# Performance work log

Hardware: AMD Instinct MI355X
Metric: run time of the kernel (lower is better)

## Reference

```python
import jax, jax.numpy as jnp
import numpy as np

B, S, DIM = 4, 4096, 1024
BASE_COUPLING = 0.1
NUM_CYCLES = 3


def _gelu(x):
    # torch nn.GELU default = exact erf formulation
    return jax.nn.gelu(x, approximate=False)


def setup_inputs() -> dict:
    key = jax.random.key(0)
    ks = jax.random.split(key, 9)
    d = DIM

    def w(k, fan_in, fan_out):
        return (jax.random.normal(k, (fan_in, fan_out), dtype=jnp.float32)
                / np.sqrt(fan_in).astype(np.float32))

    inp = {"x": jax.random.normal(ks[0], (B, S, d), dtype=jnp.float32)}
    # coupling_net: dim -> dim -> dim/2 -> dim/4 -> 1
    cn_dims = [(d, d), (d, d // 2), (d // 2, d // 4), (d // 4, 1)]
    for i, (a, b) in enumerate(cn_dims):
        inp[f"cn_w{i+1}"] = w(ks[1 + i], a, b)
        inp[f"cn_b{i+1}"] = jnp.zeros((b,), dtype=jnp.float32)
    # global_context_net: dim -> dim/2 -> dim/4 -> 1
    gc_dims = [(d, d // 2), (d // 2, d // 4), (d // 4, 1)]
    for i, (a, b) in enumerate(gc_dims):
        inp[f"gc_w{i+1}"] = w(ks[5 + i], a, b)
        inp[f"gc_b{i+1}"] = jnp.zeros((b,), dtype=jnp.float32)
    inp["adaptive_range"] = jnp.full((1,), 0.2, dtype=jnp.float32)
    return inp


def _coupling_net(h, w1, b1, w2, b2, w3, b3, w4, b4):
    h = _gelu(h @ w1 + b1)
    h = _gelu(h @ w2 + b2)
    h = _gelu(h @ w3 + b3)
    return jax.nn.sigmoid(h @ w4 + b4)  # [..., 1]


def _global_net(h, w1, b1, w2, b2, w3, b3):
    h = _gelu(h @ w1 + b1)
    h = _gelu(h @ w2 + b2)
    return jax.nn.sigmoid(h @ w3 + b3)  # [b, 1, 1]


def _twist(x):
    # x: [b, s, dim]; omega = first half, pi = second half;
    # each split again into real/imag halves -> quarters [or, oi, pr, pim].
    # omega_new = [pr, -pim], pi_new = [-or, oi]  (position-independent elementwise swap)
    o_r, o_i, p_r, p_i = jnp.split(x, 4, axis=-1)
    return jnp.concatenate([p_r, -p_i, -o_r, o_i], axis=-1)


def reference(x, cn_w1, cn_b1, cn_w2, cn_b2, cn_w3, cn_b3, cn_w4, cn_b4,
              gc_w1, gc_b1, gc_w2, gc_b2, gc_w3, gc_b3, adaptive_range):
    global_context = x.mean(axis=1, keepdims=True)  # [b, 1, dim]
    gf = _global_net(global_context, gc_w1, gc_b1, gc_w2, gc_b2, gc_w3, gc_b3)  # [b,1,1]
    out = x
    for _ in range(NUM_CYCLES):
        tf = _coupling_net(out, cn_w1, cn_b1, cn_w2, cn_b2, cn_w3, cn_b3, cn_w4, cn_b4)  # [b,s,1]
        combined = 0.7 * gf + 0.3 * tf
        coupling = BASE_COUPLING + adaptive_range * (combined - 0.5) * 2.0  # [b,s,1]
        out = out + coupling * _twist(out)
    return out
```

## Files before the change

kernel.cpp:

```cpp
#include <hip/hip_runtime.h>
#include <hip/hip_bf16.h>

#define PB 4
#define PS 4096
#define PD 1024
#define ROWS (PB * PS)
#define NUM_CYCLES 3
#define BASE_COUPLING 0.1f

typedef __attribute__((ext_vector_type(8))) short bf16x8;
typedef __attribute__((ext_vector_type(4))) float f32x4;

__device__ __forceinline__ float geluf(float x) {
    return 0.5f * x * (1.0f + erff(x * 0.70710678118654752440f));
}
__device__ __forceinline__ float gelu_fast(float x) {
    float u = (x + 0.044715f * x * x * x) * 2.3022077f;
    return x * __builtin_amdgcn_rcpf(1.0f + exp2f(-u));
}
__device__ __forceinline__ float sigmf_(float x) {
    return 1.0f / (1.0f + expf(-x));
}
__device__ __forceinline__ uint2 pk4(float4 v) {
    __hip_bfloat16 h[4] = {__float2bfloat16(v.x), __float2bfloat16(v.y),
                           __float2bfloat16(v.z), __float2bfloat16(v.w)};
    return *reinterpret_cast<uint2*>(h);
}
__device__ __forceinline__ float4 axpy4(float4 a, float s, float4 b) {
    return make_float4(fmaf(s, b.x, a.x), fmaf(s, b.y, a.y),
                       fmaf(s, b.z, a.z), fmaf(s, b.w, a.w));
}
__device__ __forceinline__ float bf2f(unsigned short u) {
    unsigned int w = ((unsigned int)u) << 16;
    return __builtin_bit_cast(float, w);
}
__device__ __forceinline__ float4 ubf2f4(uint2 u) {
    unsigned short h[4];
    *reinterpret_cast<uint2*>(h) = u;
    return make_float4(bf2f(h[0]), bf2f(h[1]), bf2f(h[2]), bf2f(h[3]));
}

#define GLD_LDS16(gsrc, ldst)                                                        \
    __builtin_amdgcn_global_load_lds(                                                \
        (const __attribute__((address_space(1))) void*)(gsrc),                       \
        (__attribute__((address_space(3))) void*)(ldst), 16, 0, 0)

__global__ __launch_bounds__(256) void copy_cvt_kernel(const float* __restrict__ x,
                                                       __hip_bfloat16* __restrict__ outb,
                                                       int n4) {
    int stride = gridDim.x * blockDim.x;
    for (int i = blockIdx.x * blockDim.x + threadIdx.x; i < n4; i += stride) {
        float4 v = reinterpret_cast<const float4*>(x)[i];
        reinterpret_cast<uint2*>(outb)[i] = pk4(v);
    }
}

__global__ __launch_bounds__(256) void mean_stage1(const __hip_bfloat16* __restrict__ xb,
                                                   float* __restrict__ part) {
    int b = blockIdx.x >> 6, sc = blockIdx.x & 63;
    size_t base = ((size_t)b * PS + (size_t)sc * 64) * PD;
    const uint2* x2 = reinterpret_cast<const uint2*>(xb + base);
    int t = threadIdx.x;
    float4 acc = make_float4(0.f, 0.f, 0.f, 0.f);
    for (int r = 0; r < 64; ++r) {
        float4 v = ubf2f4(x2[r * 256 + t]);
        acc.x += v.x; acc.y += v.y; acc.z += v.z; acc.w += v.w;
    }
    reinterpret_cast<float4*>(part + ((size_t)(b * 64 + sc)) * PD)[t] = acc;
}

__global__ __launch_bounds__(256) void mean_stage2(const float* __restrict__ part,
                                                   float* __restrict__ gc) {
    int b = blockIdx.x, t = threadIdx.x;
    float4 s = make_float4(0.f, 0.f, 0.f, 0.f);
    for (int c = 0; c < 64; ++c) {
        float4 v = reinterpret_cast<const float4*>(part + ((size_t)(b * 64 + c)) * PD)[t];
        s.x += v.x; s.y += v.y; s.z += v.z; s.w += v.w;
    }
    s.x *= (1.0f / 4096.0f); s.y *= (1.0f / 4096.0f);
    s.z *= (1.0f / 4096.0f); s.w *= (1.0f / 4096.0f);
    reinterpret_cast<float4*>(gc + (size_t)b * PD)[t] = s;
}

__global__ __launch_bounds__(256) void transpose_w_kernel(const float* __restrict__ W,
                                                          __hip_bfloat16* __restrict__ Wt,
                                                          int K, int N) {
    __shared__ float t[32][33];
    int k0 = blockIdx.x * 32, n0 = blockIdx.y * 32;
    int tx = threadIdx.x & 31, ty = threadIdx.x >> 5;
#pragma unroll
    for (int i = 0; i < 32; i += 8)
        t[ty + i][tx] = W[(size_t)(k0 + ty + i) * N + n0 + tx];
    __syncthreads();
#pragma unroll
    for (int i = 0; i < 32; i += 8)
        Wt[(size_t)(n0 + ty + i) * K + k0 + tx] = __float2bfloat16(t[tx][ty + i]);
}

__global__ __launch_bounds__(256) void gn1_kernel(const float* __restrict__ gc,
                                                  const float* __restrict__ w1,
                                                  const float* __restrict__ b1,
                                                  float* __restrict__ g1) {
    __shared__ float gcs[1024];
    __shared__ float red[4][64];
    int b = blockIdx.x, j0 = blockIdx.y * 64;
    int t = threadIdx.x, wave = t >> 6, lane = t & 63;
    for (int i = t; i < 1024; i += 256) gcs[i] = gc[(size_t)b * PD + i];
    __syncthreads();
    int j = j0 + lane;
    float a = 0.f;
    int k0 = wave * 256;
    for (int k = k0; k < k0 + 256; ++k) a += gcs[k] * w1[(size_t)k * 512 + j];
    red[wave][lane] = a;
    __syncthreads();
    if (wave == 0) {
        float v = red[0][lane] + red[1][lane] + red[2][lane] + red[3][lane] + b1[j];
        g1[(size_t)b * 512 + j] = geluf(v);
    }
}

__global__ __launch_bounds__(256) void gn2_kernel(const float* __restrict__ g1,
                                                  const float* __restrict__ w2,
                                                  const float* __restrict__ b2,
                                                  float* __restrict__ g2) {
    __shared__ float g1s[512];
    __shared__ float red[4][64];
    int b = blockIdx.x, j0 = blockIdx.y * 64;
    int t = threadIdx.x, wave = t >> 6, lane = t & 63;
    for (int i = t; i < 512; i += 256) g1s[i] = g1[(size_t)b * 512 + i];
    __syncthreads();
    int j = j0 + lane;
    float a = 0.f;
    int k0 = wave * 128;
    for (int k = k0; k < k0 + 128; ++k) a += g1s[k] * w2[(size_t)k * 256 + j];
    red[wave][lane] = a;
    __syncthreads();
    if (wave == 0) {
        float v = red[0][lane] + red[1][lane] + red[2][lane] + red[3][lane] + b2[j];
        g2[(size_t)b * 256 + j] = geluf(v);
    }
}

__global__ __launch_bounds__(256) void gn3_kernel(const float* __restrict__ g2,
                                                  const float* __restrict__ w3,
                                                  const float* __restrict__ b3,
                                                  float* __restrict__ gf) {
    __shared__ float red[256];
    int b = blockIdx.x, t = threadIdx.x;
    red[t] = g2[(size_t)b * 256 + t] * w3[t];
    __syncthreads();
    for (int s = 128; s > 0; s >>= 1) {
        if (t < s) red[t] += red[t + s];
        __syncthreads();
    }
    if (t == 0) gf[b] = sigmf_(red[0] + b3[0]);
}

__global__ __launch_bounds__(256, 2) void gemm128b64_kernel(
    const __hip_bfloat16* __restrict__ A,
    const __hip_bfloat16* __restrict__ Wt,
    const float* __restrict__ bias,
    __hip_bfloat16* __restrict__ C,
    int K, int N) {
    __shared__ __align__(16) __hip_bfloat16 Als[2][128 * 64];
    __shared__ __align__(16) __hip_bfloat16 Bls[2][128 * 64];
    const int tid = threadIdx.x;
    const int wave = tid >> 6, lane = tid & 63;
    const int m0 = blockIdx.x * 128, n0 = blockIdx.y * 128;
    const int wr = wave >> 1, wc = wave & 1;
    const int fr = lane & 15, fq = lane >> 4;

    int sr[4], sk[4], sbb[4];
#pragma unroll
    for (int j = 0; j < 4; ++j) {
        int c = wave * 64 + j * 256 + lane;
        int P = c * 16;
        int L = P ^ (((P >> 7) & 7) << 4);
        sr[j] = L >> 7;
        sk[j] = (L & 127) >> 1;
        sbb[j] = (wave * 64 + j * 256) * 16;
    }
    int abyte[4], bbyte[4];
#pragma unroll
    for (int f = 0; f < 4; ++f) {
        int rowA = wr * 64 + f * 16 + fr;
        abyte[f] = (rowA * 128 + fq * 16) ^ ((rowA & 7) << 4);
        int rowB = wc * 64 + f * 16 + fr;
        bbyte[f] = (rowB * 128 + fq * 16) ^ ((rowB & 7) << 4);
    }

    f32x4 acc[4][4] = {};
    bf16x8 av[4][2], bv[4][2];

#define STAGE(bufn, kt) do {                                                         \
    _Pragma("unroll") for (int j = 0; j < 4; ++j) {                                  \
        GLD_LDS16(A + (size_t)(m0 + sr[j]) * K + (kt) + sk[j], (char*)Als[bufn] + sbb[j]); \
        GLD_LDS16(Wt + (size_t)(n0 + sr[j]) * K + (kt) + sk[j], (char*)Bls[bufn] + sbb[j]); \
    }                                                                                \
} while (0)

    STAGE(0, 0);
    __syncthreads();

    const int nt = K >> 6;
    for (int t = 0; t < nt; ++t) {
        const int buf = t & 1;
#pragma unroll
        for (int ni = 0; ni < 4; ++ni)
#pragma unroll
            for (int kk = 0; kk < 2; ++kk)
                bv[ni][kk] = *(const bf16x8*)((const char*)&Bls[buf][0] + (bbyte[ni] ^ (kk << 6)));
#pragma unroll
        for (int mi = 0; mi < 4; ++mi)
#pragma unroll
            for (int kk = 0; kk < 2; ++kk)
                av[mi][kk] = *(const bf16x8*)((const char*)&Als[buf][0] + (abyte[mi] ^ (kk << 6)));
        if (t + 1 < nt) STAGE(buf ^ 1, (t + 1) << 6);
        __builtin_amdgcn_s_setprio(1);
#pragma unroll
        for (int kk = 0; kk < 2; ++kk)
#pragma unroll
            for (int mi = 0; mi < 4; ++mi)
#pragma unroll
                for (int ni = 0; ni < 4; ++ni)
                    acc[mi][ni] = __builtin_amdgcn_mfma_f32_16x16x32_bf16(
                        av[mi][kk], bv[ni][kk], acc[mi][ni], 0, 0, 0);
        __builtin_amdgcn_s_setprio(0);
        __syncthreads();
    }

#pragma unroll
    for (int mi = 0; mi < 4; ++mi) {
#pragma unroll
        for (int ni = 0; ni < 4; ++ni) {
            int n = n0 + wc * 64 + ni * 16 + fr;
            float bs = bias[n];
#pragma unroll
            for (int r = 0; r < 4; ++r) {
                int m = m0 + wr * 64 + mi * 16 + fq * 4 + r;
                C[(size_t)m * N + n] = __float2bfloat16(gelu_fast(acc[mi][ni][r] + bs));
            }
        }
    }
#undef STAGE
}

__global__ __launch_bounds__(256, 2) void gemm128b64_pdot_kernel(
    const __hip_bfloat16* __restrict__ A,
    const __hip_bfloat16* __restrict__ Wt,
    const float* __restrict__ bias,
    const float* __restrict__ w4,
    float* __restrict__ pdot,
    int K, int N) {
    __shared__ __align__(16) __hip_bfloat16 Als[2][128 * 64];
    __shared__ __align__(16) __hip_bfloat16 Bls[2][128 * 64];
    __shared__ float spd[128][2];
    const int tid = threadIdx.x;
    const int wave = tid >> 6, lane = tid & 63;
    const int m0 = blockIdx.x * 128, n0 = blockIdx.y * 128;
    const int nb = blockIdx.y;
    const int wr = wave >> 1, wc = wave & 1;
    const int fr = lane & 15, fq = lane >> 4;

    int sr[4], sk[4], sbb[4];
#pragma unroll
    for (int j = 0; j < 4; ++j) {
        int c = wave * 64 + j * 256 + lane;
        int P = c * 16;
        int L = P ^ (((P >> 7) & 7) << 4);
        sr[j] = L >> 7;
        sk[j] = (L & 127) >> 1;
        sbb[j] = (wave * 64 + j * 256) * 16;
    }
    int abyte[4], bbyte[4];
#pragma unroll
    for (int f = 0; f < 4; ++f) {
        int rowA = wr * 64 + f * 16 + fr;
        abyte[f] = (rowA * 128 + fq * 16) ^ ((rowA & 7) << 4);
        int rowB = wc * 64 + f * 16 + fr;
        bbyte[f] = (rowB * 128 + fq * 16) ^ ((rowB & 7) << 4);
    }

    f32x4 acc[4][4] = {};
    bf16x8 av[4][2], bv[4][2];

#define STAGE(bufn, kt) do {                                                         \
    _Pragma("unroll") for (int j = 0; j < 4; ++j) {                                  \
        GLD_LDS16(A + (size_t)(m0 + sr[j]) * K + (kt) + sk[j], (char*)Als[bufn] + sbb[j]); \
        GLD_LDS16(Wt + (size_t)(n0 + sr[j]) * K + (kt) + sk[j], (char*)Bls[bufn] + sbb[j]); \
    }                                                                                \
} while (0)

    STAGE(0, 0);
    __syncthreads();

    const int nt = K >> 6;
    for (int t = 0; t < nt; ++t) {
        const int buf = t & 1;
#pragma unroll
        for (int ni = 0; ni < 4; ++ni)
#pragma unroll
            for (int kk = 0; kk < 2; ++kk)
                bv[ni][kk] = *(const bf16x8*)((const char*)&Bls[buf][0] + (bbyte[ni] ^ (kk << 6)));
#pragma unroll
        for (int mi = 0; mi < 4; ++mi)
#pragma unroll
            for (int kk = 0; kk < 2; ++kk)
                av[mi][kk] = *(const bf16x8*)((const char*)&Als[buf][0] + (abyte[mi] ^ (kk << 6)));
        if (t + 1 < nt) STAGE(buf ^ 1, (t + 1) << 6);
        __builtin_amdgcn_s_setprio(1);
#pragma unroll
        for (int kk = 0; kk < 2; ++kk)
#pragma unroll
            for (int mi = 0; mi < 4; ++mi)
#pragma unroll
                for (int ni = 0; ni < 4; ++ni)
                    acc[mi][ni] = __builtin_amdgcn_mfma_f32_16x16x32_bf16(
                        av[mi][kk], bv[ni][kk], acc[mi][ni], 0, 0, 0);
        __builtin_amdgcn_s_setprio(0);
        __syncthreads();
    }

    float pd[4][4];
#pragma unroll
    for (int mi = 0; mi < 4; ++mi)
#pragma unroll
        for (int r = 0; r < 4; ++r) {
            float s = 0.f;
#pragma unroll
            for (int ni = 0; ni < 4; ++ni) {
                int n = n0 + wc * 64 + ni * 16 + fr;
                s += gelu_fast(acc[mi][ni][r] + bias[n]) * w4[n];
            }
            pd[mi][r] = s;
        }
#pragma unroll
    for (int off = 1; off < 16; off <<= 1)
#pragma unroll
        for (int mi = 0; mi < 4; ++mi)
#pragma unroll
            for (int r = 0; r < 4; ++r)
                pd[mi][r] += __shfl_xor(pd[mi][r], off);
    if (fr == 0) {
#pragma unroll
        for (int mi = 0; mi < 4; ++mi)
#pragma unroll
            for (int r = 0; r < 4; ++r)
                spd[wr * 64 + mi * 16 + fq * 4 + r][wc] = pd[mi][r];
    }
    __syncthreads();
    if (tid < 128) pdot[(size_t)(m0 + tid) * 2 + nb] = spd[tid][0] + spd[tid][1];
#undef STAGE
}

__global__ __launch_bounds__(256) void tf_update_kernel(
    const float* __restrict__ srcf, const __hip_bfloat16* __restrict__ srcb, int use_bf,
    const float* __restrict__ pdot,
    const float* __restrict__ b4,
    const float* __restrict__ gf, const float* __restrict__ arp,
    float* __restrict__ out, __hip_bfloat16* __restrict__ outb, int wf, int wb) {
    const int wid = threadIdx.x >> 6, lane = threadIdx.x & 63;
    const int r = blockIdx.x * 4 + wid;
    const int b = r >> 12;

    float2 pv = reinterpret_cast<const float2*>(pdot)[r];
    float tf = sigmf_(pv.x + pv.y + b4[0]);
    float comb = 0.7f * gf[b] + 0.3f * tf;
    float c = BASE_COUPLING + arp[0] * (comb - 0.5f) * 2.0f;

    float4 o_r, o_i, p_r, p_i;
    if (use_bf) {
        const uint2* s2 = reinterpret_cast<const uint2*>(srcb + (size_t)r * PD);
        o_r = ubf2f4(s2[lane]);
        o_i = ubf2f4(s2[64 + lane]);
        p_r = ubf2f4(s2[128 + lane]);
        p_i = ubf2f4(s2[192 + lane]);
    } else {
        const float4* s4 = reinterpret_cast<const float4*>(srcf + (size_t)r * PD);
        o_r = s4[lane];
        o_i = s4[64 + lane];
        p_r = s4[128 + lane];
        p_i = s4[192 + lane];
    }
    float4 n0 = axpy4(o_r, c, p_r);
    float4 n1 = axpy4(o_i, -c, p_i);
    float4 n2 = axpy4(p_r, -c, o_r);
    float4 n3 = axpy4(p_i, c, o_i);
    if (wf) {
        float4* row4 = reinterpret_cast<float4*>(out + (size_t)r * PD);
        row4[lane] = n0;
        row4[64 + lane] = n1;
        row4[128 + lane] = n2;
        row4[192 + lane] = n3;
    }
    if (wb) {
        uint2* rb4 = reinterpret_cast<uint2*>(outb + (size_t)r * PD);
        rb4[lane] = pk4(n0);
        rb4[64 + lane] = pk4(n1);
        rb4[128 + lane] = pk4(n2);
        rb4[192 + lane] = pk4(n3);
    }
}

extern "C" void kernel_launch(void* const* d_in, const int* in_sizes, int n_in,
                              void* d_out, int out_size, void* d_ws, size_t ws_size,
                              hipStream_t stream) {
    const float* x     = (const float*)d_in[0];
    const float* cn_w1 = (const float*)d_in[1];
    const float* cn_b1 = (const float*)d_in[2];
    const float* cn_w2 = (const float*)d_in[3];
    const float* cn_b2 = (const float*)d_in[4];
    const float* cn_w3 = (const float*)d_in[5];
    const float* cn_b3 = (const float*)d_in[6];
    const float* cn_w4 = (const float*)d_in[7];
    const float* cn_b4 = (const float*)d_in[8];
    const float* gc_w1 = (const float*)d_in[9];
    const float* gc_b1 = (const float*)d_in[10];
    const float* gc_w2 = (const float*)d_in[11];
    const float* gc_b2 = (const float*)d_in[12];
    const float* gc_w3 = (const float*)d_in[13];
    const float* gc_b3 = (const float*)d_in[14];
    const float* ar    = (const float*)d_in[15];

    float* out = (float*)d_out;

    char* ws = (char*)d_ws;
    __hip_bfloat16* h1   = (__hip_bfloat16*)(ws);
    __hip_bfloat16* h2   = (__hip_bfloat16*)(ws + ((size_t)32 << 20));
    __hip_bfloat16* outb = (__hip_bfloat16*)(ws + ((size_t)56 << 20));
    __hip_bfloat16* wt1  = (__hip_bfloat16*)(ws + ((size_t)88 << 20));
    __hip_bfloat16* wt2  = (__hip_bfloat16*)(ws + ((size_t)90 << 20));
    __hip_bfloat16* wt3  = (__hip_bfloat16*)(ws + ((size_t)91 << 20));
    float* pdot          = (float*)(ws + ((size_t)91 << 20) + (1 << 18));
    float* part          = (float*)(ws + ((size_t)91 << 20) + (3 << 17));
    float* gc            = part + 4 * 64 * PD;
    float* g1            = gc + 4 * PD;
    float* g2            = g1 + 4 * 512;
    float* gf            = g2 + 4 * 256;

    transpose_w_kernel<<<dim3(32, 32), 256, 0, stream>>>(cn_w1, wt1, 1024, 1024);
    transpose_w_kernel<<<dim3(32, 16), 256, 0, stream>>>(cn_w2, wt2, 1024, 512);
    transpose_w_kernel<<<dim3(16, 8), 256, 0, stream>>>(cn_w3, wt3, 512, 256);

    copy_cvt_kernel<<<2048, 256, 0, stream>>>(x, outb, ROWS * PD / 4);
    mean_stage1<<<256, 256, 0, stream>>>(outb, part);
    mean_stage2<<<PB, 256, 0, stream>>>(part, gc);

    gn1_kernel<<<dim3(PB, 8), 256, 0, stream>>>(gc, gc_w1, gc_b1, g1);
    gn2_kernel<<<dim3(PB, 4), 256, 0, stream>>>(g1, gc_w2, gc_b2, g2);
    gn3_kernel<<<PB, 256, 0, stream>>>(g2, gc_w3, gc_b3, gf);

    for (int cyc = 0; cyc < NUM_CYCLES; ++cyc) {
        gemm128b64_kernel<<<dim3(128, 8), 256, 0, stream>>>(outb, wt1, cn_b1, h1, 1024, 1024);
        gemm128b64_kernel<<<dim3(128, 4), 256, 0, stream>>>(h1, wt2, cn_b2, h2, 1024, 512);
        gemm128b64_pdot_kernel<<<dim3(128, 2), 256, 0, stream>>>(h2, wt3, cn_b3, cn_w4, pdot, 512, 256);
        int last = (cyc + 1 == NUM_CYCLES);
        tf_update_kernel<<<ROWS / 4, 256, 0, stream>>>(
            x, outb, (cyc > 0) ? 1 : 0, pdot, cn_b4, gf, ar,
            out, outb, last ? 1 : 0, last ? 0 : 1);
    }
}
```

Baseline: 326.2 us.

## Switch GEMMs to 256x128 tiles with K=32 steps and unified templated kernel

Replaces the 128x128 tile, K=64 GEMM kernels with a single templated 256x128 tile kernel using K=32 per stage, with a new LDS swizzle and split A-fragment loads between MFMA batches. Larger M tiles raise the arithmetic intensity per loaded B element and halve the grid, while the smaller K step keeps LDS usage similar. The cost is 128 accumulator floats per thread, which raises register pressure and may lower occupancy. Grid count drops to 512/256/128 blocks, which could underfill 256 CUs for the smaller GEMMs.

```diff
diff --git a/kernel.cpp b/kernel.cpp
--- a/kernel.cpp
+++ b/kernel.cpp
@@ -156,200 +156,148 @@
     if (t == 0) gf[b] = sigmf_(red[0] + b3[0]);
 }
 
-__global__ __launch_bounds__(256, 2) void gemm128b64_kernel(
-    const __hip_bfloat16* __restrict__ A,
-    const __hip_bfloat16* __restrict__ Wt,
-    const float* __restrict__ bias,
-    __hip_bfloat16* __restrict__ C,
-    int K, int N) {
-    __shared__ __align__(16) __hip_bfloat16 Als[2][128 * 64];
-    __shared__ __align__(16) __hip_bfloat16 Bls[2][128 * 64];
-    const int tid = threadIdx.x;
-    const int wave = tid >> 6, lane = tid & 63;
-    const int m0 = blockIdx.x * 128, n0 = blockIdx.y * 128;
-    const int wr = wave >> 1, wc = wave & 1;
-    const int fr = lane & 15, fq = lane >> 4;
-
-    int sr[4], sk[4], sbb[4];
-#pragma unroll
-    for (int j = 0; j < 4; ++j) {
-        int c = wave * 64 + j * 256 + lane;
-        int P = c * 16;
-        int L = P ^ (((P >> 7) & 7) << 4);
-        sr[j] = L >> 7;
-        sk[j] = (L & 127) >> 1;
-        sbb[j] = (wave * 64 + j * 256) * 16;
-    }
-    int abyte[4], bbyte[4];
-#pragma unroll
-    for (int f = 0; f < 4; ++f) {
-        int rowA = wr * 64 + f * 16 + fr;
-        abyte[f] = (rowA * 128 + fq * 16) ^ ((rowA & 7) << 4);
-        int rowB = wc * 64 + f * 16 + fr;
-        bbyte[f] = (rowB * 128 + fq * 16) ^ ((rowB & 7) << 4);
-    }
-
-    f32x4 acc[4][4] = {};
-    bf16x8 av[4][2], bv[4][2];
-
-#define STAGE(bufn, kt) do {                                                         \
-    _Pragma("unroll") for (int j = 0; j < 4; ++j) {                                  \
-        GLD_LDS16(A + (size_t)(m0 + sr[j]) * K + (kt) + sk[j], (char*)Als[bufn] + sbb[j]); \
-        GLD_LDS16(Wt + (size_t)(n0 + sr[j]) * K + (kt) + sk[j], (char*)Bls[bufn] + sbb[j]); \
-    }                                                                                \
-} while (0)
-
-    STAGE(0, 0);
-    __syncthreads();
-
-    const int nt = K >> 6;
-    for (int t = 0; t < nt; ++t) {
-        const int buf = t & 1;
-#pragma unroll
-        for (int ni = 0; ni < 4; ++ni)
-#pragma unroll
-            for (int kk = 0; kk < 2; ++kk)
-                bv[ni][kk] = *(const bf16x8*)((const char*)&Bls[buf][0] + (bbyte[ni] ^ (kk << 6)));
-#pragma unroll
-        for (int mi = 0; mi < 4; ++mi)
-#pragma unroll
-            for (int kk = 0; kk < 2; ++kk)
-                av[mi][kk] = *(const bf16x8*)((const char*)&Als[buf][0] + (abyte[mi] ^ (kk << 6)));
-        if (t + 1 < nt) STAGE(buf ^ 1, (t + 1) << 6);
-        __builtin_amdgcn_s_setprio(1);
-#pragma unroll
-        for (int kk = 0; kk < 2; ++kk)
-#pragma unroll
-            for (int mi = 0; mi < 4; ++mi)
-#pragma unroll
-                for (int ni = 0; ni < 4; ++ni)
-                    acc[mi][ni] = __builtin_amdgcn_mfma_f32_16x16x32_bf16(
-                        av[mi][kk], bv[ni][kk], acc[mi][ni], 0, 0, 0);
-        __builtin_amdgcn_s_setprio(0);
-        __syncthreads();
-    }
-
-#pragma unroll
-    for (int mi = 0; mi < 4; ++mi) {
-#pragma unroll
-        for (int ni = 0; ni < 4; ++ni) {
-            int n = n0 + wc * 64 + ni * 16 + fr;
-            float bs = bias[n];
-#pragma unroll
-            for (int r = 0; r < 4; ++r) {
-                int m = m0 + wr * 64 + mi * 16 + fq * 4 + r;
-                C[(size_t)m * N + n] = __float2bfloat16(gelu_fast(acc[mi][ni][r] + bs));
-            }
-        }
-    }
-#undef STAGE
-}
-
-__global__ __launch_bounds__(256, 2) void gemm128b64_pdot_kernel(
+template <int EPI>
+__global__ __launch_bounds__(256, 2) void gemm256x128_kernel(
     const __hip_bfloat16* __restrict__ A,
     const __hip_bfloat16* __restrict__ Wt,
     const float* __restrict__ bias,
     const float* __restrict__ w4,
+    __hip_bfloat16* __restrict__ C,
     float* __restrict__ pdot,
     int K, int N) {
-    __shared__ __align__(16) __hip_bfloat16 Als[2][128 * 64];
-    __shared__ __align__(16) __hip_bfloat16 Bls[2][128 * 64];
-    __shared__ float spd[128][2];
+    __shared__ __align__(16) __hip_bfloat16 Als[2][256 * 32];
+    __shared__ __align__(16) __hip_bfloat16 Bls[2][128 * 32];
+    __shared__ float spd[EPI ? 256 : 1][2];
     const int tid = threadIdx.x;
     const int wave = tid >> 6, lane = tid & 63;
-    const int m0 = blockIdx.x * 128, n0 = blockIdx.y * 128;
-    const int nb = blockIdx.y;
+    const int m0 = blockIdx.x * 256, n0 = blockIdx.y * 128;
     const int wr = wave >> 1, wc = wave & 1;
     const int fr = lane & 15, fq = lane >> 4;
 
-    int sr[4], sk[4], sbb[4];
+    int sAr[4], sAk[4], sAb[4];
 #pragma unroll
     for (int j = 0; j < 4; ++j) {
-        int c = wave * 64 + j * 256 + lane;
+        int c = j * 256 + wave * 64 + lane;
         int P = c * 16;
-        int L = P ^ (((P >> 7) & 7) << 4);
-        sr[j] = L >> 7;
-        sk[j] = (L & 127) >> 1;
-        sbb[j] = (wave * 64 + j * 256) * 16;
-    }
-    int abyte[4], bbyte[4];
-#pragma unroll
-    for (int f = 0; f < 4; ++f) {
-        int rowA = wr * 64 + f * 16 + fr;
-        abyte[f] = (rowA * 128 + fq * 16) ^ ((rowA & 7) << 4);
-        int rowB = wc * 64 + f * 16 + fr;
-        bbyte[f] = (rowB * 128 + fq * 16) ^ ((rowB & 7) << 4);
-    }
-
-    f32x4 acc[4][4] = {};
-    bf16x8 av[4][2], bv[4][2];
-
-#define STAGE(bufn, kt) do {                                                         \
-    _Pragma("unroll") for (int j = 0; j < 4; ++j) {                                  \
-        GLD_LDS16(A + (size_t)(m0 + sr[j]) * K + (kt) + sk[j], (char*)Als[bufn] + sbb[j]); \
-        GLD_LDS16(Wt + (size_t)(n0 + sr[j]) * K + (kt) + sk[j], (char*)Bls[bufn] + sbb[j]); \
-    }                                                                                \
+        int row = P >> 6;
+        int off = (P & 63) ^ (((row >> 1) & 3) << 4);
+        sAr[j] = row;
+        sAk[j] = off >> 1;
+        sAb[j] = (j * 256 + wave * 64) * 16;
+    }
+    int sBr[2], sBk[2], sBb[2];
+#pragma unroll
+    for (int j = 0; j < 2; ++j) {
+        int c = j * 256 + wave * 64 + lane;
+        int P = c * 16;
+        int row = P >> 6;
+        int off = (P & 63) ^ (((row >> 1) & 3) << 4);
+        sBr[j] = row;
+        sBk[j] = off >> 1;
+        sBb[j] = (j * 256 + wave * 64) * 16;
+    }
+    int abyte[8], bbyte[4];
+#pragma unroll
+    for (int fm = 0; fm < 8; ++fm) {
+        int row = wr * 128 + fm * 16 + fr;
+        abyte[fm] = (row * 64 + fq * 16) ^ (((row >> 1) & 3) << 4);
+    }
+#pragma unroll
+    for (int fn = 0; fn < 4; ++fn) {
+        int row = wc * 64 + fn * 16 + fr;
+        bbyte[fn] = (row * 64 + fq * 16) ^ (((row >> 1) & 3) << 4);
+    }
+
+    f32x4 acc[8][4] = {};
+    bf16x8 av[4], bv[4];
+
+#define STAGE(bufn, kt) do {                                                          \
+    _Pragma("unroll") for (int j = 0; j < 4; ++j)                                     \
+        GLD_LDS16(A + (size_t)(m0 + sAr[j]) * K + (kt) + sAk[j], (char*)Als[bufn] + sAb[j]); \
+    _Pragma("unroll") for (int j = 0; j < 2; ++j)                                     \
+        GLD_LDS16(Wt + (size_t)(n0 + sBr[j]) * K + (kt) + sBk[j], (char*)Bls[bufn] + sBb[j]); \
 } while (0)
 
     STAGE(0, 0);
     __syncthreads();
 
-    const int nt = K >> 6;
+    const int nt = K >> 5;
     for (int t = 0; t < nt; ++t) {
         const int buf = t & 1;
 #pragma unroll
         for (int ni = 0; ni < 4; ++ni)
-#pragma unroll
-            for (int kk = 0; kk < 2; ++kk)
-                bv[ni][kk] = *(const bf16x8*)((const char*)&Bls[buf][0] + (bbyte[ni] ^ (kk << 6)));
+            bv[ni] = *(const bf16x8*)((const char*)&Bls[buf][0] + bbyte[ni]);
 #pragma unroll
         for (int mi = 0; mi < 4; ++mi)
-#pragma unroll
-            for (int kk = 0; kk < 2; ++kk)
-                av[mi][kk] = *(const bf16x8*)((const char*)&Als[buf][0] + (abyte[mi] ^ (kk << 6)));
-        if (t + 1 < nt) STAGE(buf ^ 1, (t + 1) << 6);
+            av[mi] = *(const bf16x8*)((const char*)&Als[buf][0] + abyte[mi]);
+        if (t + 1 < nt) STAGE(buf ^ 1, (t + 1) << 5);
         __builtin_amdgcn_s_setprio(1);
 #pragma unroll
-        for (int kk = 0; kk < 2; ++kk)
-#pragma unroll
-            for (int mi = 0; mi < 4; ++mi)
-#pragma unroll
-                for (int ni = 0; ni < 4; ++ni)
-                    acc[mi][ni] = __builtin_amdgcn_mfma_f32_16x16x32_bf16(
-                        av[mi][kk], bv[ni][kk], acc[mi][ni], 0, 0, 0);
+        for (int mi = 0; mi < 4; ++mi)
+#pragma unroll
+            for (int ni = 0; ni < 4; ++ni)
+                acc[mi][ni] = __builtin_amdgcn_mfma_f32_16x16x32_bf16(
+                    av[mi], bv[ni], acc[mi][ni], 0, 0, 0);
+        __builtin_amdgcn_s_setprio(0);
+#pragma unroll
+        for (int mi = 0; mi < 4; ++mi)
+            av[mi] = *(const bf16x8*)((const char*)&Als[buf][0] + abyte[4 + mi]);
+        __builtin_amdgcn_s_setprio(1);
+#pragma unroll
+        for (int mi = 0; mi < 4; ++mi)
+#pragma unroll
+            for (int ni = 0; ni < 4; ++ni)
+                acc[4 + mi][ni] = __builtin_amdgcn_mfma_f32_16x16x32_bf16(
+                    av[mi], bv[ni], acc[4 + mi][ni], 0, 0, 0);
         __builtin_amdgcn_s_setprio(0);
         __syncthreads();
     }
 
-    float pd[4][4];
-#pragma unroll
-    for (int mi = 0; mi < 4; ++mi)
-#pragma unroll
-        for (int r = 0; r < 4; ++r) {
-            float s = 0.f;
-#pragma unroll
-            for (int ni = 0; ni < 4; ++ni) {
-                int n = n0 + wc * 64 + ni * 16 + fr;
-                s += gelu_fast(acc[mi][ni][r] + bias[n]) * w4[n];
+    if (EPI == 0) {
+#pragma unroll
+        for (int fm = 0; fm < 8; ++fm) {
+#pragma unroll
+            for (int fn = 0; fn < 4; ++fn) {
+                int n = n0 + wc * 64 + fn * 16 + fr;
+                float bs = bias[n];
+#pragma unroll
+                for (int r = 0; r < 4; ++r) {
+                    int m = m0 + wr * 128 + fm * 16 + fq * 4 + r;
+                    C[(size_t)m * N + n] = __float2bfloat16(gelu_fast(acc[fm][fn][r] + bs));
+                }
             }
-            pd[mi][r] = s;
         }
-#pragma unroll
-    for (int off = 1; off < 16; off <<= 1)
-#pragma unroll
-        for (int mi = 0; mi < 4; ++mi)
-#pragma unroll
-            for (int r = 0; r < 4; ++r)
-                pd[mi][r] += __shfl_xor(pd[mi][r], off);
-    if (fr == 0) {
-#pragma unroll
-        for (int mi = 0; mi < 4; ++mi)
-#pragma unroll
-            for (int r = 0; r < 4; ++r)
-                spd[wr * 64 + mi * 16 + fq * 4 + r][wc] = pd[mi][r];
-    }
-    __syncthreads();
-    if (tid < 128) pdot[(size_t)(m0 + tid) * 2 + nb] = spd[tid][0] + spd[tid][1];
+    } else {
+        float pd[8][4];
+#pragma unroll
+        for (int fm = 0; fm < 8; ++fm)
+#pragma unroll
+            for (int r = 0; r < 4; ++r) {
+                float s = 0.f;
+#pragma unroll
+                for (int fn = 0; fn < 4; ++fn) {
+                    int n = n0 + wc * 64 + fn * 16 + fr;
+                    s += gelu_fast(acc[fm][fn][r] + bias[n]) * w4[n];
+                }
+                pd[fm][r] = s;
+            }
+#pragma unroll
+        for (int off = 1; off < 16; off <<= 1)
+#pragma unroll
+            for (int fm = 0; fm < 8; ++fm)
+#pragma unroll
+                for (int r = 0; r < 4; ++r)
+                    pd[fm][r] += __shfl_xor(pd[fm][r], off);
+        if (fr == 0) {
+#pragma unroll
+            for (int fm = 0; fm < 8; ++fm)
+#pragma unroll
+                for (int r = 0; r < 4; ++r)
+                    spd[wr * 128 + fm * 16 + fq * 4 + r][wc] = pd[fm][r];
+        }
+        __syncthreads();
+        pdot[(size_t)(m0 + tid) * 2 + blockIdx.y] = spd[tid][0] + spd[tid][1];
+    }
 #undef STAGE
 }
 
@@ -451,9 +399,12 @@
     gn3_kernel<<<PB, 256, 0, stream>>>(g2, gc_w3, gc_b3, gf);
 
     for (int cyc = 0; cyc < NUM_CYCLES; ++cyc) {
-        gemm128b64_kernel<<<dim3(128, 8), 256, 0, stream>>>(outb, wt1, cn_b1, h1, 1024, 1024);
-        gemm128b64_kernel<<<dim3(128, 4), 256, 0, stream>>>(h1, wt2, cn_b2, h2, 1024, 512);
-        gemm128b64_pdot_kernel<<<dim3(128, 2), 256, 0, stream>>>(h2, wt3, cn_b3, cn_w4, pdot, 512, 256);
+        gemm256x128_kernel<0><<<dim3(64, 8), 256, 0, stream>>>(
+            outb, wt1, cn_b1, nullptr, h1, nullptr, 1024, 1024);
+        gemm256x128_kernel<0><<<dim3(64, 4), 256, 0, stream>>>(
+            h1, wt2, cn_b2, nullptr, h2, nullptr, 1024, 512);
+        gemm256x128_kernel<1><<<dim3(64, 2), 256, 0, stream>>>(
+            h2, wt3, cn_b3, cn_w4, nullptr, pdot, 512, 256);
         int last = (cyc + 1 == NUM_CYCLES);
         tf_update_kernel<<<ROWS / 4, 256, 0, stream>>>(
             x, outb, (cyc > 0) ? 1 : 0, pdot, cn_b4, gf, ar,
```

New measurement: 365.3 us. 1.12x slower.

## Use 256x256-tile 8-wave GEMM with interleaved staged prefetch for first layer

Applied to the files above, without the earlier changes.

Replaces the first coupling-net GEMM (16384x1024x1024) with a new kernel using 256x256 output tiles, 512 threads (8 waves), and an XOR-swizzled LDS layout. Global-to-LDS loads for the next K tile are split into four stages interleaved with MFMA quarters, using explicit vmcnt waits and barriers. MFMA sections run at raised wave priority, and block IDs are swizzled for L2 locality. Larger tiles raise arithmetic intensity, at the cost of one block per CU, only 256 blocks, and hand-tuned wait counts that are fragile.

```diff
diff --git a/kernel.cpp b/kernel.cpp
--- a/kernel.cpp
+++ b/kernel.cpp
@@ -44,6 +44,13 @@
     __builtin_amdgcn_global_load_lds(                                                \
         (const __attribute__((address_space(1))) void*)(gsrc),                       \
         (__attribute__((address_space(3))) void*)(ldst), 16, 0, 0)
+
+#define ASM_VMCNT4() asm volatile("s_waitcnt vmcnt(4)" ::: "memory")
+#define ASM_VMCNT2() asm volatile("s_waitcnt vmcnt(2)" ::: "memory")
+#define ASM_VMCNT0() asm volatile("s_waitcnt vmcnt(0)" ::: "memory")
+#define ASM_LGKM0()  asm volatile("s_waitcnt lgkmcnt(0)" ::: "memory")
+#define SCHED_FENCE() __builtin_amdgcn_sched_barrier(0)
+#define BAR() __builtin_amdgcn_s_barrier()
 
 __global__ __launch_bounds__(256) void copy_cvt_kernel(const float* __restrict__ x,
                                                        __hip_bfloat16* __restrict__ outb,
@@ -154,6 +161,139 @@
         __syncthreads();
     }
     if (t == 0) gf[b] = sigmf_(red[0] + b3[0]);
+}
+
+__global__ __launch_bounds__(512, 1) void gemm8p_kernel(
+    const __hip_bfloat16* __restrict__ A,
+    const __hip_bfloat16* __restrict__ Wt,
+    const float* __restrict__ bias,
+    __hip_bfloat16* __restrict__ C,
+    int K, int N) {
+    __shared__ __align__(16) __hip_bfloat16 Als[2][256 * 64];
+    __shared__ __align__(16) __hip_bfloat16 Bls[2][256 * 64];
+    const int tid = threadIdx.x;
+    const int wave = tid >> 6, lane = tid & 63;
+    const int nbn = N >> 8;
+    const int nwg = gridDim.x;
+    const int bid = blockIdx.x;
+    const int swz = (bid & 7) * (nwg >> 3) + (bid >> 3);
+    const int m0 = (swz / nbn) * 256, n0 = (swz % nbn) * 256;
+    const int wr = wave >> 2, wc = wave & 3;
+    const int fr = lane & 15, fq = lane >> 4;
+
+    int srcoff[4][2], cb[4][2];
+#pragma unroll
+    for (int r = 0; r < 2; ++r) {
+        int binrow = (lane & 7) * 16;
+        int rowA0 = r * 128 + ((wave * 64 + lane) >> 3);
+        int rowA1 = 64 + rowA0;
+        int g = r * 2 + (wave >> 2);
+        int cc = (wave & 3) * 64 + lane;
+        int rowB0 = g * 64 + (cc >> 3);
+        int rowB1 = rowB0 + 32;
+        int kA0 = (binrow ^ ((rowA0 & 7) << 4)) >> 1;
+        int kA1 = (binrow ^ ((rowA1 & 7) << 4)) >> 1;
+        int kB0 = (binrow ^ ((rowB0 & 7) << 4)) >> 1;
+        int kB1 = (binrow ^ ((rowB1 & 7) << 4)) >> 1;
+        srcoff[0][r] = (m0 + rowA0) * K + kA0;
+        srcoff[1][r] = (n0 + rowB0) * K + kB0;
+        srcoff[2][r] = (n0 + rowB1) * K + kB1;
+        srcoff[3][r] = (m0 + rowA1) * K + kA1;
+        cb[0][r] = r * 16384 + wave * 1024;
+        cb[1][r] = g * 8192 + (wave & 3) * 1024;
+        cb[2][r] = g * 8192 + 4096 + (wave & 3) * 1024;
+        cb[3][r] = 8192 + r * 16384 + wave * 1024;
+    }
+    int abyte[8], bbyte[4];
+#pragma unroll
+    for (int fm = 0; fm < 8; ++fm) {
+        int row = wr * 128 + fm * 16 + fr;
+        abyte[fm] = (row * 128 + fq * 16) ^ ((row & 7) << 4);
+    }
+#pragma unroll
+    for (int fn = 0; fn < 4; ++fn) {
+        int row = wc * 64 + fn * 16 + fr;
+        bbyte[fn] = (row * 128 + fq * 16) ^ ((row & 7) << 4);
+    }
+
+    f32x4 acc[8][4] = {};
+    bf16x8 av[4][2], bv01[2][2], bv23[2][2];
+
+#define STG(u, bufn, kt) do {                                                        \
+    const __hip_bfloat16* sb_ = ((u) == 0 || (u) == 3) ? A : Wt;                     \
+    __hip_bfloat16* lb_ = ((u) == 0 || (u) == 3) ? &Als[bufn][0] : &Bls[bufn][0];    \
+    GLD_LDS16(sb_ + srcoff[u][0] + (kt), (char*)lb_ + cb[u][0]);                     \
+    GLD_LDS16(sb_ + srcoff[u][1] + (kt), (char*)lb_ + cb[u][1]);                     \
+} while (0)
+
+#define RD_A(BUF, H)                                                                 \
+    _Pragma("unroll") for (int mi = 0; mi < 4; ++mi)                                 \
+      _Pragma("unroll") for (int kk = 0; kk < 2; ++kk)                               \
+        av[mi][kk] = *(const bf16x8*)((const char*)&Als[BUF][0] + (abyte[(H)*4 + mi] ^ (kk << 6)));
+#define RD_B(BUF, H, DST)                                                            \
+    _Pragma("unroll") for (int ni = 0; ni < 2; ++ni)                                 \
+      _Pragma("unroll") for (int kk = 0; kk < 2; ++kk)                               \
+        DST[ni][kk] = *(const bf16x8*)((const char*)&Bls[BUF][0] + (bbyte[(H)*2 + ni] ^ (kk << 6)));
+#define MFMAQ(MH, NH, BV)                                                            \
+    __builtin_amdgcn_s_setprio(1);                                                   \
+    _Pragma("unroll") for (int kk = 0; kk < 2; ++kk)                                 \
+      _Pragma("unroll") for (int mi = 0; mi < 4; ++mi)                               \
+        _Pragma("unroll") for (int ni = 0; ni < 2; ++ni)                             \
+          acc[(MH)*4 + mi][(NH)*2 + ni] = __builtin_amdgcn_mfma_f32_16x16x32_bf16(   \
+              av[mi][kk], BV[ni][kk], acc[(MH)*4 + mi][(NH)*2 + ni], 0, 0, 0);       \
+    __builtin_amdgcn_s_setprio(0);
+
+    STG(0, 0, 0); STG(1, 0, 0); STG(2, 0, 0); STG(3, 0, 0);
+    ASM_VMCNT0();
+    BAR();
+
+    const int nt = K >> 6;
+    for (int t = 0; t < nt; ++t) {
+        const int buf = t & 1;
+        const int nbuf = buf ^ 1;
+        const int ktn = (t + 1) << 6;
+        const bool pf = (t + 1 < nt);
+        RD_A(buf, 0);
+        RD_B(buf, 0, bv01);
+        if (pf) STG(0, nbuf, ktn);
+        ASM_LGKM0(); SCHED_FENCE();
+        MFMAQ(0, 0, bv01);
+        if (pf) ASM_VMCNT4(); else ASM_VMCNT2();
+        BAR();
+        RD_B(buf, 1, bv23);
+        if (pf) STG(1, nbuf, ktn);
+        ASM_LGKM0(); SCHED_FENCE();
+        MFMAQ(0, 1, bv23);
+        if (pf) ASM_VMCNT4(); else ASM_VMCNT0();
+        BAR();
+        RD_A(buf, 1);
+        if (pf) STG(2, nbuf, ktn);
+        ASM_LGKM0(); SCHED_FENCE();
+        MFMAQ(1, 1, bv23);
+        BAR();
+        if (pf) STG(3, nbuf, ktn);
+        MFMAQ(1, 0, bv01);
+        if (pf) ASM_VMCNT4();
+        BAR();
+    }
+
+#pragma unroll
+    for (int fm = 0; fm < 8; ++fm) {
+#pragma unroll
+        for (int fn = 0; fn < 4; ++fn) {
+            int n = n0 + wc * 64 + fn * 16 + fr;
+            float bs = bias[n];
+#pragma unroll
+            for (int r = 0; r < 4; ++r) {
+                int m = m0 + wr * 128 + fm * 16 + fq * 4 + r;
+                C[(size_t)m * N + n] = __float2bfloat16(gelu_fast(acc[fm][fn][r] + bs));
+            }
+        }
+    }
+#undef STG
+#undef RD_A
+#undef RD_B
+#undef MFMAQ
 }
 
 __global__ __launch_bounds__(256, 2) void gemm128b64_kernel(
@@ -451,7 +591,7 @@
     gn3_kernel<<<PB, 256, 0, stream>>>(g2, gc_w3, gc_b3, gf);
 
     for (int cyc = 0; cyc < NUM_CYCLES; ++cyc) {
-        gemm128b64_kernel<<<dim3(128, 8), 256, 0, stream>>>(outb, wt1, cn_b1, h1, 1024, 1024);
+        gemm8p_kernel<<<64 * 4, 512, 0, stream>>>(outb, wt1, cn_b1, h1, 1024, 1024);
         gemm128b64_kernel<<<dim3(128, 4), 256, 0, stream>>>(h1, wt2, cn_b2, h2, 1024, 512);
         gemm128b64_pdot_kernel<<<dim3(128, 2), 256, 0, stream>>>(h2, wt3, cn_b3, cn_w4, pdot, 512, 256);
         int last = (cyc + 1 == NUM_CYCLES);
```

New measurement: 322.8 us. About the same (-1.0%).

## Run the first two coupling-net GEMMs in FP8 e4m3 with scaled weights

Applied to the files above, without the earlier changes.

Weights W1 and W2 are transposed and quantized to FP8 e4m3 with a fixed scale of 256. Activations are also written in FP8, both by a new fused kernel that converts x and computes the mean partials in one pass, and by the update kernel. The first two GEMMs now use the fp8 16x16x32 MFMA with 64-byte swizzled LDS rows, which halves operand traffic and raises matrix throughput. The first GEMM writes FP8 and the second writes bf16 for the last layer. The cost is lower numerical precision in the coupling-network path, plus extra per-element conversion work in software.

```diff
diff --git a/kernel.cpp b/kernel.cpp
--- a/kernel.cpp
+++ b/kernel.cpp
@@ -7,6 +7,8 @@
 #define ROWS (PB * PS)
 #define NUM_CYCLES 3
 #define BASE_COUPLING 0.1f
+#define WSCALE 256.0f
+#define INV_WSCALE (1.0f / 256.0f)
 
 typedef __attribute__((ext_vector_type(8))) short bf16x8;
 typedef __attribute__((ext_vector_type(4))) float f32x4;
@@ -39,42 +41,58 @@
     *reinterpret_cast<uint2*>(h) = u;
     return make_float4(bf2f(h[0]), bf2f(h[1]), bf2f(h[2]), bf2f(h[3]));
 }
+__device__ __forceinline__ unsigned char f2e4m3(float x) {
+    unsigned int u = __builtin_bit_cast(unsigned int, x);
+    unsigned int s = (u >> 24) & 0x80u;
+    float ax = __builtin_fabsf(x);
+    if (!(ax >= 0.015625f)) return (unsigned char)s;
+    if (ax >= 464.0f) return (unsigned char)(s | 0x7Eu);
+    unsigned int au = u & 0x7FFFFFFFu;
+    unsigned int lsb = (au >> 20) & 1u;
+    au += 0x0007FFFFu + lsb;
+    unsigned int e = (au >> 23) - 127u + 7u;
+    unsigned int m = (au >> 20) & 7u;
+    if (e >= 16u) return (unsigned char)(s | 0x7Eu);
+    return (unsigned char)(s | (e << 3) | m);
+}
+__device__ __forceinline__ unsigned int pk8(float4 v) {
+    return (unsigned int)f2e4m3(v.x) | ((unsigned int)f2e4m3(v.y) << 8) |
+           ((unsigned int)f2e4m3(v.z) << 16) | ((unsigned int)f2e4m3(v.w) << 24);
+}
 
 #define GLD_LDS16(gsrc, ldst)                                                        \
     __builtin_amdgcn_global_load_lds(                                                \
         (const __attribute__((address_space(1))) void*)(gsrc),                       \
         (__attribute__((address_space(3))) void*)(ldst), 16, 0, 0)
 
-__global__ __launch_bounds__(256) void copy_cvt_kernel(const float* __restrict__ x,
-                                                       __hip_bfloat16* __restrict__ outb,
-                                                       int n4) {
-    int stride = gridDim.x * blockDim.x;
-    for (int i = blockIdx.x * blockDim.x + threadIdx.x; i < n4; i += stride) {
-        float4 v = reinterpret_cast<const float4*>(x)[i];
-        reinterpret_cast<uint2*>(outb)[i] = pk4(v);
-    }
-}
-
-__global__ __launch_bounds__(256) void mean_stage1(const __hip_bfloat16* __restrict__ xb,
-                                                   float* __restrict__ part) {
-    int b = blockIdx.x >> 6, sc = blockIdx.x & 63;
-    size_t base = ((size_t)b * PS + (size_t)sc * 64) * PD;
-    const uint2* x2 = reinterpret_cast<const uint2*>(xb + base);
+#define ASM_VMCNT4() asm volatile("s_waitcnt vmcnt(4)" ::: "memory")
+#define ASM_VMCNT0() asm volatile("s_waitcnt vmcnt(0)" ::: "memory")
+#define ASM_LGKM0()  asm volatile("s_waitcnt lgkmcnt(0)" ::: "memory")
+#define SCHED_FENCE() __builtin_amdgcn_sched_barrier(0)
+
+__global__ __launch_bounds__(256) void copy_mean_cvt_kernel(const float* __restrict__ x,
+                                                            unsigned char* __restrict__ outb8,
+                                                            float* __restrict__ part) {
+    int b = blockIdx.x >> 7, sc = blockIdx.x & 127;
+    size_t base = ((size_t)b * PS + (size_t)sc * 32) * PD;
+    const float4* x4 = reinterpret_cast<const float4*>(x + base);
+    unsigned int* o8 = reinterpret_cast<unsigned int*>(outb8 + base);
     int t = threadIdx.x;
     float4 acc = make_float4(0.f, 0.f, 0.f, 0.f);
-    for (int r = 0; r < 64; ++r) {
-        float4 v = ubf2f4(x2[r * 256 + t]);
+    for (int r = 0; r < 32; ++r) {
+        float4 v = x4[r * 256 + t];
+        o8[r * 256 + t] = pk8(v);
         acc.x += v.x; acc.y += v.y; acc.z += v.z; acc.w += v.w;
     }
-    reinterpret_cast<float4*>(part + ((size_t)(b * 64 + sc)) * PD)[t] = acc;
+    reinterpret_cast<float4*>(part + ((size_t)(b * 128 + sc)) * PD)[t] = acc;
 }
 
 __global__ __launch_bounds__(256) void mean_stage2(const float* __restrict__ part,
                                                    float* __restrict__ gc) {
     int b = blockIdx.x, t = threadIdx.x;
     float4 s = make_float4(0.f, 0.f, 0.f, 0.f);
-    for (int c = 0; c < 64; ++c) {
-        float4 v = reinterpret_cast<const float4*>(part + ((size_t)(b * 64 + c)) * PD)[t];
+    for (int c = 0; c < 128; ++c) {
+        float4 v = reinterpret_cast<const float4*>(part + ((size_t)(b * 128 + c)) * PD)[t];
         s.x += v.x; s.y += v.y; s.z += v.z; s.w += v.w;
     }
     s.x *= (1.0f / 4096.0f); s.y *= (1.0f / 4096.0f);
@@ -95,6 +113,21 @@
 #pragma unroll
     for (int i = 0; i < 32; i += 8)
         Wt[(size_t)(n0 + ty + i) * K + k0 + tx] = __float2bfloat16(t[tx][ty + i]);
+}
+
+__global__ __launch_bounds__(256) void transpose_w8_kernel(const float* __restrict__ W,
+                                                           unsigned char* __restrict__ Wt8,
+                                                           int K, int N) {
+    __shared__ float t[32][33];
+    int k0 = blockIdx.x * 32, n0 = blockIdx.y * 32;
+    int tx = threadIdx.x & 31, ty = threadIdx.x >> 5;
+#pragma unroll
+    for (int i = 0; i < 32; i += 8)
+        t[ty + i][tx] = W[(size_t)(k0 + ty + i) * N + n0 + tx];
+    __syncthreads();
+#pragma unroll
+    for (int i = 0; i < 32; i += 8)
+        Wt8[(size_t)(n0 + ty + i) * K + k0 + tx] = f2e4m3(t[tx][ty + i] * WSCALE);
 }
 
 __global__ __launch_bounds__(256) void gn1_kernel(const float* __restrict__ gc,
@@ -156,75 +189,81 @@
     if (t == 0) gf[b] = sigmf_(red[0] + b3[0]);
 }
 
-__global__ __launch_bounds__(256, 2) void gemm128b64_kernel(
-    const __hip_bfloat16* __restrict__ A,
-    const __hip_bfloat16* __restrict__ Wt,
+template <int OUTFP8>
+__global__ __launch_bounds__(256, 2) void gemm128f8_kernel(
+    const unsigned char* __restrict__ A,
+    const unsigned char* __restrict__ Wt,
     const float* __restrict__ bias,
-    __hip_bfloat16* __restrict__ C,
+    unsigned char* __restrict__ C8,
+    __hip_bfloat16* __restrict__ Cb,
     int K, int N) {
-    __shared__ __align__(16) __hip_bfloat16 Als[2][128 * 64];
-    __shared__ __align__(16) __hip_bfloat16 Bls[2][128 * 64];
+    __shared__ __align__(16) unsigned char Als[2][128 * 64];
+    __shared__ __align__(16) unsigned char Bls[2][128 * 64];
     const int tid = threadIdx.x;
     const int wave = tid >> 6, lane = tid & 63;
     const int m0 = blockIdx.x * 128, n0 = blockIdx.y * 128;
     const int wr = wave >> 1, wc = wave & 1;
     const int fr = lane & 15, fq = lane >> 4;
 
-    int sr[4], sk[4], sbb[4];
-#pragma unroll
-    for (int j = 0; j < 4; ++j) {
-        int c = wave * 64 + j * 256 + lane;
-        int P = c * 16;
-        int L = P ^ (((P >> 7) & 7) << 4);
-        sr[j] = L >> 7;
-        sk[j] = (L & 127) >> 1;
-        sbb[j] = (wave * 64 + j * 256) * 16;
-    }
-    int abyte[4], bbyte[4];
+    int sr[2], skel[2], sbase[2];
+#pragma unroll
+    for (int j = 0; j < 2; ++j) {
+        int c = j * 256 + tid;
+        int row = c >> 2;
+        int inner = (c & 3) * 16;
+        skel[j] = inner ^ ((row & 6) << 3);
+        sr[j] = row;
+        sbase[j] = (j * 256 + wave * 64) * 16;
+    }
+    int aoff[4], boff[4];
 #pragma unroll
     for (int f = 0; f < 4; ++f) {
-        int rowA = wr * 64 + f * 16 + fr;
-        abyte[f] = (rowA * 128 + fq * 16) ^ ((rowA & 7) << 4);
-        int rowB = wc * 64 + f * 16 + fr;
-        bbyte[f] = (rowB * 128 + fq * 16) ^ ((rowB & 7) << 4);
+        int rA = wr * 64 + f * 16 + fr;
+        aoff[f] = rA * 64 + ((fq * 8) ^ ((rA & 6) << 3));
+        int rB = wc * 64 + f * 16 + fr;
+        boff[f] = rB * 64 + ((fq * 8) ^ ((rB & 6) << 3));
     }
 
     f32x4 acc[4][4] = {};
-    bf16x8 av[4][2], bv[4][2];
-
-#define STAGE(bufn, kt) do {                                                         \
-    _Pragma("unroll") for (int j = 0; j < 4; ++j) {                                  \
-        GLD_LDS16(A + (size_t)(m0 + sr[j]) * K + (kt) + sk[j], (char*)Als[bufn] + sbb[j]); \
-        GLD_LDS16(Wt + (size_t)(n0 + sr[j]) * K + (kt) + sk[j], (char*)Bls[bufn] + sbb[j]); \
-    }                                                                                \
+    long av[4], bv[4];
+
+#define STAGE8(bufn, kt) do {                                                         \
+    _Pragma("unroll") for (int j = 0; j < 2; ++j) {                                   \
+        GLD_LDS16(A + (size_t)(m0 + sr[j]) * K + (kt) + skel[j], (char*)Als[bufn] + sbase[j]); \
+        GLD_LDS16(Wt + (size_t)(n0 + sr[j]) * K + (kt) + skel[j], (char*)Bls[bufn] + sbase[j]); \
+    }                                                                                 \
 } while (0)
 
-    STAGE(0, 0);
+    STAGE8(0, 0);
     __syncthreads();
 
     const int nt = K >> 6;
     for (int t = 0; t < nt; ++t) {
         const int buf = t & 1;
 #pragma unroll
-        for (int ni = 0; ni < 4; ++ni)
-#pragma unroll
-            for (int kk = 0; kk < 2; ++kk)
-                bv[ni][kk] = *(const bf16x8*)((const char*)&Bls[buf][0] + (bbyte[ni] ^ (kk << 6)));
+        for (int f = 0; f < 4; ++f) bv[f] = *(const long*)(&Bls[buf][boff[f]]);
+#pragma unroll
+        for (int f = 0; f < 4; ++f) av[f] = *(const long*)(&Als[buf][aoff[f]]);
+        if (t + 1 < nt) STAGE8(buf ^ 1, (t + 1) << 6);
+        __builtin_amdgcn_s_setprio(1);
 #pragma unroll
         for (int mi = 0; mi < 4; ++mi)
 #pragma unroll
-            for (int kk = 0; kk < 2; ++kk)
-                av[mi][kk] = *(const bf16x8*)((const char*)&Als[buf][0] + (abyte[mi] ^ (kk << 6)));
-        if (t + 1 < nt) STAGE(buf ^ 1, (t + 1) << 6);
+            for (int ni = 0; ni < 4; ++ni)
+                acc[mi][ni] = __builtin_amdgcn_mfma_f32_16x16x32_fp8_fp8(
+                    av[mi], bv[ni], acc[mi][ni], 0, 0, 0);
+        __builtin_amdgcn_s_setprio(0);
+#pragma unroll
+        for (int f = 0; f < 4; ++f) bv[f] = *(const long*)(&Bls[buf][boff[f] ^ 32]);
+#pragma unroll
+        for (int f = 0; f < 4; ++f) av[f] = *(const long*)(&Als[buf][aoff[f] ^ 32]);
         __builtin_amdgcn_s_setprio(1);
 #pragma unroll
-        for (int kk = 0; kk < 2; ++kk)
-#pragma unroll
-            for (int mi = 0; mi < 4; ++mi)
-#pragma unroll
-                for (int ni = 0; ni < 4; ++ni)
-                    acc[mi][ni] = __builtin_amdgcn_mfma_f32_16x16x32_bf16(
-                        av[mi][kk], bv[ni][kk], acc[mi][ni], 0, 0, 0);
+        for (int mi = 0; mi < 4; ++mi)
+#pragma unroll
+            for (int ni = 0; ni < 4; ++ni)
+                acc[mi][ni] = __builtin_amdgcn_mfma_f32_16x16x32_fp8_fp8(
+                    av[mi], bv[ni], acc[mi][ni], 0, 0, 0);
         __builtin_amdgcn_s_setprio(0);
         __syncthreads();
     }
@@ -238,11 +277,13 @@
 #pragma unroll
             for (int r = 0; r < 4; ++r) {
                 int m = m0 + wr * 64 + mi * 16 + fq * 4 + r;
-                C[(size_t)m * N + n] = __float2bfloat16(gelu_fast(acc[mi][ni][r] + bs));
+                float v = gelu_fast(fmaf(acc[mi][ni][r], INV_WSCALE, bs));
+                if (OUTFP8) C8[(size_t)m * N + n] = f2e4m3(v);
+                else        Cb[(size_t)m * N + n] = __float2bfloat16(v);
             }
         }
     }
-#undef STAGE
+#undef STAGE8
 }
 
 __global__ __launch_bounds__(256, 2) void gemm128b64_pdot_kernel(
@@ -358,7 +399,8 @@
     const float* __restrict__ pdot,
     const float* __restrict__ b4,
     const float* __restrict__ gf, const float* __restrict__ arp,
-    float* __restrict__ out, __hip_bfloat16* __restrict__ outb, int wf, int wb) {
+    float* __restrict__ out, __hip_bfloat16* __restrict__ outb,
+    unsigned char* __restrict__ outb8, int wf, int wb, int w8) {
     const int wid = threadIdx.x >> 6, lane = threadIdx.x & 63;
     const int r = blockIdx.x * 4 + wid;
     const int b = r >> 12;
@@ -399,6 +441,13 @@
         rb4[64 + lane] = pk4(n1);
         rb4[128 + lane] = pk4(n2);
         rb4[192 + lane] = pk4(n3);
+    }
+    if (w8) {
+        unsigned int* r8 = reinterpret_cast<unsigned int*>(outb8 + (size_t)r * PD);
+        r8[lane] = pk8(n0);
+        r8[64 + lane] = pk8(n1);
+        r8[128 + lane] = pk8(n2);
+        r8[192 + lane] = pk8(n3);
     }
 }
 
@@ -425,25 +474,25 @@
     float* out = (float*)d_out;
 
     char* ws = (char*)d_ws;
-    __hip_bfloat16* h1   = (__hip_bfloat16*)(ws);
-    __hip_bfloat16* h2   = (__hip_bfloat16*)(ws + ((size_t)32 << 20));
-    __hip_bfloat16* outb = (__hip_bfloat16*)(ws + ((size_t)56 << 20));
-    __hip_bfloat16* wt1  = (__hip_bfloat16*)(ws + ((size_t)88 << 20));
-    __hip_bfloat16* wt2  = (__hip_bfloat16*)(ws + ((size_t)90 << 20));
-    __hip_bfloat16* wt3  = (__hip_bfloat16*)(ws + ((size_t)91 << 20));
-    float* pdot          = (float*)(ws + ((size_t)91 << 20) + (1 << 18));
-    float* part          = (float*)(ws + ((size_t)91 << 20) + (3 << 17));
-    float* gc            = part + 4 * 64 * PD;
-    float* g1            = gc + 4 * PD;
-    float* g2            = g1 + 4 * 512;
-    float* gf            = g2 + 4 * 256;
-
-    transpose_w_kernel<<<dim3(32, 32), 256, 0, stream>>>(cn_w1, wt1, 1024, 1024);
-    transpose_w_kernel<<<dim3(32, 16), 256, 0, stream>>>(cn_w2, wt2, 1024, 512);
+    unsigned char* h1_8   = (unsigned char*)(ws);
+    __hip_bfloat16* h2    = (__hip_bfloat16*)(ws + ((size_t)16 << 20));
+    __hip_bfloat16* outb  = (__hip_bfloat16*)(ws + ((size_t)32 << 20));
+    unsigned char* outb8  = (unsigned char*)(ws + ((size_t)64 << 20));
+    unsigned char* wt1_8  = (unsigned char*)(ws + ((size_t)80 << 20));
+    unsigned char* wt2_8  = (unsigned char*)(ws + ((size_t)81 << 20));
+    __hip_bfloat16* wt3   = (__hip_bfloat16*)(ws + ((size_t)81 << 20) + ((size_t)1 << 19));
+    float* pdot           = (float*)(ws + ((size_t)82 << 20));
+    float* part           = (float*)(ws + ((size_t)83 << 20));
+    float* gc             = (float*)(ws + ((size_t)85 << 20));
+    float* g1             = gc + 4 * PD;
+    float* g2             = g1 + 4 * 512;
+    float* gf             = g2 + 4 * 256;
+
+    transpose_w8_kernel<<<dim3(32, 32), 256, 0, stream>>>(cn_w1, wt1_8, 1024, 1024);
+    transpose_w8_kernel<<<dim3(32, 16), 256, 0, stream>>>(cn_w2, wt2_8, 1024, 512);
     transpose_w_kernel<<<dim3(16, 8), 256, 0, stream>>>(cn_w3, wt3, 512, 256);
 
-    copy_cvt_kernel<<<2048, 256, 0, stream>>>(x, outb, ROWS * PD / 4);
-    mean_stage1<<<256, 256, 0, stream>>>(outb, part);
+    copy_mean_cvt_kernel<<<512, 256, 0, stream>>>(x, outb8, part);
     mean_stage2<<<PB, 256, 0, stream>>>(part, gc);
 
     gn1_kernel<<<dim3(PB, 8), 256, 0, stream>>>(gc, gc_w1, gc_b1, g1);
@@ -451,12 +500,15 @@
     gn3_kernel<<<PB, 256, 0, stream>>>(g2, gc_w3, gc_b3, gf);
 
     for (int cyc = 0; cyc < NUM_CYCLES; ++cyc) {
-        gemm128b64_kernel<<<dim3(128, 8), 256, 0, stream>>>(outb, wt1, cn_b1, h1, 1024, 1024);
-        gemm128b64_kernel<<<dim3(128, 4), 256, 0, stream>>>(h1, wt2, cn_b2, h2, 1024, 512);
-        gemm128b64_pdot_kernel<<<dim3(128, 2), 256, 0, stream>>>(h2, wt3, cn_b3, cn_w4, pdot, 512, 256);
+        gemm128f8_kernel<1><<<dim3(128, 8), 256, 0, stream>>>(
+            outb8, wt1_8, cn_b1, h1_8, nullptr, 1024, 1024);
+        gemm128f8_kernel<0><<<dim3(128, 4), 256, 0, stream>>>(
+            h1_8, wt2_8, cn_b2, nullptr, h2, 1024, 512);
+        gemm128b64_pdot_kernel<<<dim3(128, 2), 256, 0, stream>>>(
+            h2, wt3, cn_b3, cn_w4, pdot, 512, 256);
         int last = (cyc + 1 == NUM_CYCLES);
         tf_update_kernel<<<ROWS / 4, 256, 0, stream>>>(
             x, outb, (cyc > 0) ? 1 : 0, pdot, cn_b4, gf, ar,
-            out, outb, last ? 1 : 0, last ? 0 : 1);
-    }
-}
+            out, outb, outb8, last ? 1 : 0, last ? 0 : 1, last ? 0 : 1);
+    }
+}
```

New measurement: 319.3 us. 1.02x faster.
